# Kernel tuning notes

Hardware: AMD Instinct MI355X
Metric: run time of the kernel (lower is better)

Reference implementation:

```python
import jax, jax.numpy as jnp
import numpy as np

SIGMA_MIN, SIGMA_MAX = 0.03, 0.35
LAMBDA_GEO = 8.0
COMPAT_SCALE = 0.1
INVALID_W = 0.05
NH, HD = 8, 64
LN_EPS = 1e-5

def _ln(x, g, b):
    m = x.mean(-1, keepdims=True)
    v = ((x - m) ** 2).mean(-1, keepdims=True)
    return (x - m) * jax.lax.rsqrt(v + LN_EPS) * g + b

def setup_inputs() -> dict:
    key = jax.random.key(0)
    ks = jax.random.split(key, 32)
    B, C, H, W = 8, 512, 32, 32
    T, S, D, SIN = 1024, 1024, 512, 512
    s = 0.02
    inp = {
        'front_feat': jax.random.normal(ks[0], (B, C, H, W), jnp.float32),
        'sat_tokens': jax.random.normal(ks[1], (B, S, SIN), jnp.float32),
        'sat_xy': jax.random.uniform(ks[2], (B, S, 2), jnp.float32),
        'front_bev_xy': jax.random.uniform(ks[3], (B, T, 2), jnp.float32),
        'front_bev_valid_mask': jax.random.bernoulli(ks[4], 0.9, (B, T)),
        'front_plucker': jax.random.normal(ks[5], (B, T, 6), jnp.float32),
        'fa_w': jax.random.normal(ks[6], (C, D), jnp.float32) * s,
        'fa_b': jnp.zeros((D,), jnp.float32),
        'fa_g': jnp.ones((D,), jnp.float32),
        'fa_lb': jnp.zeros((D,), jnp.float32),
        'sa_w': jax.random.normal(ks[7], (SIN, D), jnp.float32) * s,
        'sa_b': jnp.zeros((D,), jnp.float32),
        'sa_g': jnp.ones((D,), jnp.float32),
        'sa_lb': jnp.zeros((D,), jnp.float32),
        'q_w': jax.random.normal(ks[8], (D, D), jnp.float32) * s,
        'q_b': jnp.zeros((D,), jnp.float32),
        'k_w': jax.random.normal(ks[9], (D, D), jnp.float32) * s,
        'k_b': jnp.zeros((D,), jnp.float32),
        'v_w': jax.random.normal(ks[10], (D, D), jnp.float32) * s,
        'v_b': jnp.zeros((D,), jnp.float32),
        'pl_w1': jax.random.normal(ks[11], (6, D), jnp.float32) * s,
        'pl_b1': jnp.zeros((D,), jnp.float32),
        'pl_w2': jax.random.normal(ks[12], (D, D), jnp.float32) * s,
        'pl_b2': jnp.zeros((D,), jnp.float32),
        'sig_w': jax.random.normal(ks[13], (D, 1), jnp.float32) * s,
        'sig_b': jnp.zeros((1,), jnp.float32),
        'db_w': jax.random.normal(ks[14], (D, NH), jnp.float32) * s,
        'db_b': jnp.zeros((NH,), jnp.float32),
        'out_w': jax.random.normal(ks[15], (D, C), jnp.float32) * s,
        'out_b': jnp.zeros((C,), jnp.float32),
    }
    return inp

def _forward(front_feat, sat_tokens, sat_xy, front_bev_xy, front_plucker,
             fa_w, fa_b, fa_g, fa_lb, sa_w, sa_b, sa_g, sa_lb,
             q_w, q_b, k_w, k_b, v_w, v_b, pl_w1, pl_b1, pl_w2, pl_b2,
             sig_w, sig_b, db_w, db_b, out_w, out_b, valid_mask):
    B, C, H, W = front_feat.shape
    T = H * W
    D = NH * HD
    front_flat = front_feat.reshape(B, C, T).transpose(0, 2, 1)  # [B,T,C]
    front_embed = _ln(front_flat @ fa_w + fa_b, fa_g, fa_lb)
    pl = jax.nn.silu(front_plucker @ pl_w1 + pl_b1) @ pl_w2 + pl_b2
    context = front_embed + pl
    sat_embed = _ln(sat_tokens @ sa_w + sa_b, sa_g, sa_lb)
    def heads(x):
        return x.reshape(B, -1, NH, HD).transpose(0, 2, 1, 3)  # [B,H,N,d]
    q = heads(front_embed @ q_w + q_b)
    k = heads(sat_embed @ k_w + k_b)
    v = heads(sat_embed @ v_w + v_b)
    compat = jnp.einsum('bhtd,bhsd->bhts', q, k) / jnp.sqrt(jnp.float32(HD))
    compat = COMPAT_SCALE * compat
    sigma = SIGMA_MIN + (SIGMA_MAX - SIGMA_MIN) * jax.nn.sigmoid((context @ sig_w + sig_b)[..., 0])  # [B,T]
    dist2 = ((front_bev_xy[:, :, None, :] - sat_xy[:, None, :, :]) ** 2).sum(-1)  # [B,T,S]
    geo = -LAMBDA_GEO * dist2 / jnp.maximum(sigma[..., None] ** 2, 1e-6)
    sat_logits = compat + geo[:, None]  # [B,H,T,S]
    sat_logits = jnp.where(valid_mask[:, None, :, None], sat_logits, jnp.float32(-10000.0))
    dustbin = (context @ db_w + db_b).transpose(0, 2, 1)[..., None]  # [B,H,T,1]
    logits = jnp.concatenate([sat_logits, dustbin], axis=-1)
    probs = jax.nn.softmax(logits, axis=-1)
    sat_probs, dustbin_prob = probs[..., :-1], probs[..., -1]
    read = jnp.einsum('bhts,bhsd->bhtd', sat_probs, v)
    read = read.transpose(0, 2, 1, 3).reshape(B, T, D)
    read_feat = (read @ out_w + out_b).transpose(0, 2, 1).reshape(B, C, H, W)
    confidence = (1.0 - dustbin_prob).mean(axis=1)  # [B,T]
    conf_feat = confidence.reshape(B, 1, H, W)
    front_feat_out = front_feat + conf_feat * read_feat
    vf = valid_mask.astype(confidence.dtype)
    inv = 1.0 - vf
    invalid_conf = (confidence * inv).sum() / jnp.maximum(inv.sum(), 1.0)
    invalid_conf_loss = invalid_conf * INVALID_W
    return front_feat_out, read_feat, confidence, invalid_conf_loss

def reference(front_feat, sat_tokens, sat_xy, front_bev_xy, front_bev_valid_mask, front_plucker,
              fa_w, fa_b, fa_g, fa_lb, sa_w, sa_b, sa_g, sa_lb,
              q_w, q_b, k_w, k_b, v_w, v_b, pl_w1, pl_b1, pl_w2, pl_b2,
              sig_w, sig_b, db_w, db_b, out_w, out_b):
    return _forward(front_feat, sat_tokens, sat_xy, front_bev_xy, front_plucker,
                    fa_w, fa_b, fa_g, fa_lb, sa_w, sa_b, sa_g, sa_lb,
                    q_w, q_b, k_w, k_b, v_w, v_b, pl_w1, pl_b1, pl_w2, pl_b2,
                    sig_w, sig_b, db_w, db_b, out_w, out_b, front_bev_valid_mask)
```

## Files before the change

kernel.cpp:

```cpp
#include <hip/hip_runtime.h>

typedef unsigned short u16;
typedef __attribute__((ext_vector_type(8))) short short8;
typedef __attribute__((ext_vector_type(4))) float f32x4;

constexpr int B_  = 8;
constexpr int C_  = 512;
constexpr int T_  = 1024;
constexpr int S_  = 1024;
constexpr int D_  = 512;
constexpr int NH_ = 8;
constexpr int BT_ = B_ * T_;
constexpr float INVLN2 = 1.44269504088896340736f;
constexpr float QSCALE2 = 0.0125f * INVLN2;

__device__ __forceinline__ unsigned pack2(float lo, float hi) {
    unsigned r;
    asm("v_cvt_pk_bf16_f32 %0, %1, %2" : "=v"(r) : "v"(lo), "v"(hi));
    return r;
}
__device__ __forceinline__ u16 f2bf(float x) {
    return (u16)pack2(x, x);
}
__device__ __forceinline__ float bf2f(u16 h) {
    union { unsigned u; float f; } v; v.u = ((unsigned)h) << 16;
    return v.f;
}
__device__ __forceinline__ float fexp2(float x) {
    float r;
    asm("v_exp_f32 %0, %1" : "=v"(r) : "v"(x));
    return r;
}

typedef __attribute__((address_space(3))) unsigned int lds_u32;
typedef const __attribute__((address_space(1))) unsigned int glob_u32;
__device__ __forceinline__ void g2l16(void* l, const void* g) {
    __builtin_amdgcn_global_load_lds((glob_u32*)g, (lds_u32*)l, 16, 0, 0);
}

__device__ __forceinline__ int is_valid(const void* mask, int mode, int idx) {
    if (mode == 0) return ((const int*)mask)[idx] != 0;
    if (mode == 1) return ((const float*)mask)[idx] != 0.0f;
    return ((const unsigned char*)mask)[idx] != 0;
}

__global__ __launch_bounds__(256) void prep_k(
    const float* __restrict__ ff, const float* __restrict__ sat,
    const float* __restrict__ pl,
    const float* a0, const float* a1, const float* a2, const float* a3,
    const float* a4, const float* a5, const float* a6, u16* __restrict__ WT,
    u16* __restrict__ ffb, u16* __restrict__ satb,
    const float* __restrict__ plw1, const float* __restrict__ plb1,
    u16* __restrict__ plh,
    const unsigned* __restrict__ maskw, int* __restrict__ mode,
    float* __restrict__ scal) {
    __shared__ float tile[32][33];
    int blk = blockIdx.x, tid = threadIdx.x;
    if (blk < 4096) {
        int t0 = (blk & 31) * 32, c0 = ((blk >> 5) & 15) * 32, b = blk >> 9;
        int tx = tid & 31, ty = tid >> 5;
        const float* ip = ff + (size_t)b * C_ * T_;
        for (int i = ty; i < 32; i += 8)
            tile[i][tx] = ip[(size_t)(c0 + i) * T_ + t0 + tx];
        __syncthreads();
        u16* op = ffb + (size_t)b * T_ * C_;
        for (int i = ty; i < 32; i += 8)
            op[(size_t)(t0 + i) * C_ + c0 + tx] = f2bf(tile[tx][i]);
    } else if (blk < 5888) {
        int idx = blk - 4096;
        const float* srcs[7] = {a0, a1, a2, a3, a4, a5, a6};
        int z = idx >> 8;
        const float* src = srcs[z];
        u16* d = WT + (size_t)z * 512 * 512;
        int k0 = (idx & 15) * 32, n0 = ((idx >> 4) & 15) * 32;
        int tx = tid & 31, ty = tid >> 5;
        for (int i = ty; i < 32; i += 8)
            tile[i][tx] = src[(size_t)(k0 + i) * 512 + n0 + tx];
        __syncthreads();
        for (int i = ty; i < 32; i += 8)
            d[(size_t)(n0 + i) * 512 + k0 + tx] = f2bf(tile[tx][i]);
    } else if (blk < 7936) {
        int i = (blk - 5888) * 256 + tid;
        const float4* p = (const float4*)(sat + (size_t)i * 8);
        float4 a = p[0], b = p[1];
        uint4 o;
        o.x = pack2(a.x, a.y); o.y = pack2(a.z, a.w);
        o.z = pack2(b.x, b.y); o.w = pack2(b.z, b.w);
        *(uint4*)(satb + (size_t)i * 8) = o;
    } else if (blk < 9984) {
        int m = (blk - 7936) * 4 + (tid >> 6);
        int lane = tid & 63;
        float p6[6];
#pragma unroll
        for (int j = 0; j < 6; ++j) p6[j] = pl[(size_t)m * 6 + j];
        int n0 = lane * 8;
        float acc[8];
#pragma unroll
        for (int e = 0; e < 8; ++e) acc[e] = plb1[n0 + e];
#pragma unroll
        for (int j = 0; j < 6; ++j) {
            float4 wv0 = *(const float4*)(plw1 + j * D_ + n0);
            float4 wv1 = *(const float4*)(plw1 + j * D_ + n0 + 4);
            acc[0] += p6[j] * wv0.x; acc[1] += p6[j] * wv0.y;
            acc[2] += p6[j] * wv0.z; acc[3] += p6[j] * wv0.w;
            acc[4] += p6[j] * wv1.x; acc[5] += p6[j] * wv1.y;
            acc[6] += p6[j] * wv1.z; acc[7] += p6[j] * wv1.w;
        }
        uint4 o;
        float s0 = acc[0] / (1.0f + __expf(-acc[0]));
        float s1 = acc[1] / (1.0f + __expf(-acc[1]));
        float s2 = acc[2] / (1.0f + __expf(-acc[2]));
        float s3 = acc[3] / (1.0f + __expf(-acc[3]));
        float s4 = acc[4] / (1.0f + __expf(-acc[4]));
        float s5 = acc[5] / (1.0f + __expf(-acc[5]));
        float s6 = acc[6] / (1.0f + __expf(-acc[6]));
        float s7 = acc[7] / (1.0f + __expf(-acc[7]));
        o.x = pack2(s0, s1); o.y = pack2(s2, s3);
        o.z = pack2(s4, s5); o.w = pack2(s6, s7);
        *(uint4*)(plh + (size_t)m * D_ + n0) = o;
    } else {
        __shared__ int bad_i, bad_f;
        if (tid == 0) { bad_i = 0; bad_f = 0; }
        __syncthreads();
        for (int i = tid; i < 2048; i += 256) {
            unsigned v = maskw[i];
            if (v > 1u) bad_i = 1;
            if (v != 0u && v != 0x3f800000u) bad_f = 1;
        }
        __syncthreads();
        if (tid == 0) {
            *mode = (!bad_i) ? 0 : ((!bad_f) ? 1 : 2);
            scal[0] = 0.0f; scal[1] = 0.0f;
        }
    }
}

__global__ __launch_bounds__(256) void gmm_k(
    const u16* __restrict__ A0, const u16* __restrict__ A1,
    const u16* __restrict__ A2, const u16* __restrict__ A3,
    const u16* __restrict__ Bt0, const u16* __restrict__ Bt1,
    const u16* __restrict__ Bt2, const u16* __restrict__ Bt3,
    const float* __restrict__ bb0, const float* __restrict__ bb1,
    const float* __restrict__ bb2, const float* __restrict__ bb3,
    void* __restrict__ C0v, void* __restrict__ C1v,
    void* __restrict__ C2v, void* __restrict__ C3v,
    int md0, int md1, int md2, int md3,
    const u16* __restrict__ addend,
    const float* __restrict__ ffp, const float* __restrict__ confp,
    float* __restrict__ out1p) {
    __shared__ u16 As[2][4096];
    __shared__ u16 Bs[2][4096];
    int jid = blockIdx.x >> 8;
    int L = blockIdx.x & 255;
    const u16* A    = (jid == 0) ? A0 : (jid == 1) ? A1 : (jid == 2) ? A2 : A3;
    const u16* Bt   = (jid == 0) ? Bt0 : (jid == 1) ? Bt1 : (jid == 2) ? Bt2 : Bt3;
    const float* bias = (jid == 0) ? bb0 : (jid == 1) ? bb1 : (jid == 2) ? bb2 : bb3;
    void* Cv        = (jid == 0) ? C0v : (jid == 1) ? C1v : (jid == 2) ? C2v : C3v;
    int mode        = (jid == 0) ? md0 : (jid == 1) ? md1 : (jid == 2) ? md2 : md3;

    int tid = threadIdx.x, w = tid >> 6, l = tid & 63;
    int lr = l & 15, g = l >> 4;
    int W = (L & 7) * 32 + (L >> 3);
    int m0 = (W >> 2) * 128, n0 = (W & 3) * 128;
    int wr = w >> 1, wc = w & 1;
    int prm = g ^ ((lr >> 1) & 3);

    f32x4 acc[4][4] = {};

    auto stage = [&](int buf, int k0) {
#pragma unroll
        for (int j = 0; j < 2; ++j) {
            int i = tid + 256 * j;
            int row = i >> 2, gg = (i & 3) ^ ((i >> 3) & 3);
            g2l16((char*)As[buf] + (size_t)i * 16,
                  A + (size_t)(m0 + row) * 512 + k0 + gg * 8);
        }
#pragma unroll
        for (int j = 0; j < 2; ++j) {
            int i = tid + 256 * j;
            int col = i >> 2, gg = (i & 3) ^ ((i >> 3) & 3);
            g2l16((char*)Bs[buf] + (size_t)i * 16,
                  Bt + (size_t)(n0 + col) * 512 + k0 + gg * 8);
        }
    };

    stage(0, 0);
    __syncthreads();
    int cur = 0;
    for (int t = 0; t < 16; ++t) {
        if (t < 15) stage(cur ^ 1, (t + 1) * 32);
        const char* Ab = (const char*)As[cur];
        const char* Bb = (const char*)Bs[cur];
        short8 af[4], bf[4];
#pragma unroll
        for (int m = 0; m < 4; ++m)
            af[m] = *(const short8*)(Ab + ((wr * 64 + m * 16 + lr) * 4 + prm) * 16);
#pragma unroll
        for (int n = 0; n < 4; ++n)
            bf[n] = *(const short8*)(Bb + ((wc * 64 + n * 16 + lr) * 4 + prm) * 16);
        __builtin_amdgcn_s_setprio(1);
#pragma unroll
        for (int m = 0; m < 4; ++m)
#pragma unroll
            for (int n = 0; n < 4; ++n)
                acc[m][n] = __builtin_amdgcn_mfma_f32_16x16x32_bf16(
                    af[m], bf[n], acc[m][n], 0, 0, 0);
        __builtin_amdgcn_s_setprio(0);
        __syncthreads();
        cur ^= 1;
    }

    float bs[4];
#pragma unroll
    for (int n = 0; n < 4; ++n) bs[n] = bias[n0 + wc * 64 + n * 16 + lr];

#pragma unroll
    for (int m = 0; m < 4; ++m) {
#pragma unroll
        for (int n = 0; n < 4; ++n) {
            int R0  = m0 + wr * 64 + m * 16 + 4 * g;
            int col = n0 + wc * 64 + n * 16 + lr;
            if (mode == 3) {
                int bbx = R0 >> 10, ss = R0 & 1023, hh = col >> 6, dd = col & 63;
                uint2 pk;
                pk.x = pack2(acc[m][n][0] + bs[n], acc[m][n][1] + bs[n]);
                pk.y = pack2(acc[m][n][2] + bs[n], acc[m][n][3] + bs[n]);
                u16* dst = (u16*)Cv + ((size_t)(bbx * 8 + hh) * 64 + dd) * 1024 + ss;
                *(uint2*)dst = pk;
            } else if (mode == 4) {
                int bbx = R0 >> 10, t0p = R0 & 1023;
                size_t base = (size_t)bbx * C_ * T_ + (size_t)col * T_ + t0p;
                float4 rf;
                rf.x = acc[m][n][0] + bs[n]; rf.y = acc[m][n][1] + bs[n];
                rf.z = acc[m][n][2] + bs[n]; rf.w = acc[m][n][3] + bs[n];
                float4 ffv = *(const float4*)(ffp + base);
                float4 cfv = *(const float4*)(confp + bbx * T_ + t0p);
                float4 o0v;
                o0v.x = ffv.x + cfv.x * rf.x; o0v.y = ffv.y + cfv.y * rf.y;
                o0v.z = ffv.z + cfv.z * rf.z; o0v.w = ffv.w + cfv.w * rf.w;
                *(float4*)(out1p + base) = rf;
                *(float4*)((float*)Cv + base) = o0v;
            } else {
#pragma unroll
                for (int j = 0; j < 4; ++j) {
                    int row = R0 + j;
                    float v = acc[m][n][j] + bs[n];
                    if (mode == 1) v *= QSCALE2;
                    if (mode == 2) v += bf2f(addend[(size_t)row * 512 + col]);
                    ((u16*)Cv)[(size_t)row * 512 + col] = f2bf(v);
                }
            }
        }
    }
}

__global__ __launch_bounds__(256) void ln2_k(
    const u16* __restrict__ X0, const float* __restrict__ g0,
    const float* __restrict__ b0, u16* __restrict__ O0,
    const u16* __restrict__ X1, const float* __restrict__ g1,
    const float* __restrict__ b1, u16* __restrict__ O1) {
    int sel = blockIdx.x >> 13;
    int row = blockIdx.x & 8191;
    const u16* X = sel ? X1 : X0;
    const float* gw = sel ? g1 : g0;
    const float* bw = sel ? b1 : b0;
    u16* out = sel ? O1 : O0;
    int tid = threadIdx.x;
    const unsigned* xr = (const unsigned*)(X + (size_t)row * D_);
    unsigned u = xr[tid];
    float x0 = bf2f((u16)(u & 0xffff)), x1 = bf2f((u16)(u >> 16));
    float s = x0 + x1, sq = x0 * x0 + x1 * x1;
    __shared__ float rs[4], rq[4];
    for (int o = 32; o; o >>= 1) { s += __shfl_down(s, o); sq += __shfl_down(sq, o); }
    int wid = tid >> 6, lane = tid & 63;
    if (lane == 0) { rs[wid] = s; rq[wid] = sq; }
    __syncthreads();
    if (tid == 0) {
        float ts = 0, tq = 0;
        for (int w = 0; w < 4; ++w) { ts += rs[w]; tq += rq[w]; }
        rs[0] = ts; rq[0] = tq;
    }
    __syncthreads();
    float mean = rs[0] * (1.0f / D_);
    float var  = rq[0] * (1.0f / D_) - mean * mean;
    float r = rsqrtf(var + 1e-5f);
    float2 g2 = *(const float2*)(gw + 2 * tid);
    float2 b2 = *(const float2*)(bw + 2 * tid);
    float y0 = (x0 - mean) * r * g2.x + b2.x;
    float y1 = (x1 - mean) * r * g2.y + b2.y;
    ((unsigned*)(out + (size_t)row * D_))[tid] = pack2(y0, y1);
}

__global__ __launch_bounds__(256) void head_k(const u16* __restrict__ ctx,
        const float* __restrict__ sw, const float* __restrict__ sbb,
        const float* __restrict__ dw, const float* __restrict__ dbb,
        float* __restrict__ sig, float* __restrict__ dbo) {
    int w = threadIdx.x >> 6, lane = threadIdx.x & 63;
    int row = blockIdx.x * 4 + w;
    const u16* xr = ctx + (size_t)row * D_;
    short8 xv = *(const short8*)(xr + lane * 8);
    float xs[8];
#pragma unroll
    for (int i = 0; i < 8; ++i) xs[i] = bf2f((u16)xv[i]);
    float4 wa = *(const float4*)(sw + lane * 8);
    float4 wb = *(const float4*)(sw + lane * 8 + 4);
    float sacc = xs[0] * wa.x + xs[1] * wa.y + xs[2] * wa.z + xs[3] * wa.w +
                 xs[4] * wb.x + xs[5] * wb.y + xs[6] * wb.z + xs[7] * wb.w;
    float d_[8] = {};
    const float* dr = dw + (size_t)lane * 8 * NH_;
#pragma unroll
    for (int i = 0; i < 8; ++i)
#pragma unroll
        for (int hh = 0; hh < 8; ++hh) d_[hh] += xs[i] * dr[i * NH_ + hh];
    for (int o = 32; o; o >>= 1) {
        sacc += __shfl_down(sacc, o);
#pragma unroll
        for (int hh = 0; hh < 8; ++hh) d_[hh] += __shfl_down(d_[hh], o);
    }
    if (lane == 0) {
        float z = sacc + sbb[0];
        sig[row] = 0.03f + 0.32f / (1.0f + __expf(-z));
        float* dd = dbo + (size_t)row * NH_;
#pragma unroll
        for (int hh = 0; hh < 8; ++hh) dd[hh] = d_[hh] + dbb[hh];
    }
}

__global__ __launch_bounds__(512) void attn_k(
    const u16* __restrict__ Q, const u16* __restrict__ K,
    const u16* __restrict__ Vt, const float* __restrict__ sig,
    const float* __restrict__ dbl, const float* __restrict__ bev,
    const float* __restrict__ sxy, const void* __restrict__ mask,
    const int* __restrict__ mode, u16* __restrict__ OUT,
    float* __restrict__ dbp) {
    int L = blockIdx.x;
    int W = (L & 7) * 64 + (L >> 3);
    int b = W >> 6, h = (W >> 3) & 7, tblk = W & 7;
    int tid = threadIdx.x, w = tid >> 6, l = tid & 63;
    int lr = l & 15, g = l >> 4;
    int p8 = lr & 7;

    __shared__ u16 Kbuf[2][4096];
    __shared__ u16 Vbuf[2][4096];
    __shared__ float2 SXY[1024];
    __shared__ float  SZ[1024];

    const float2* xp = (const float2*)(sxy + (size_t)b * S_ * 2);
#pragma unroll
    for (int j = 0; j < 2; ++j) {
        int idx = tid + 512 * j;
        float2 v = xp[idx];
        SXY[idx] = make_float2(-2.0f * v.x, -2.0f * v.y);
        SZ[idx] = v.x * v.x + v.y * v.y;
    }

    int trow = b * T_ + tblk * 128 + w * 16 + lr;
    float s_ = sig[trow];
    float bx = bev[(size_t)trow * 2], by = bev[(size_t)trow * 2 + 1];
    float dbv2 = dbl[(size_t)trow * NH_ + h] * INVLN2;
    int md = *mode;
    bool vld = is_valid(mask, md, trow) != 0;
    float grow  = vld ? (-11.5415603271117f / fmaxf(s_ * s_, 1e-6f)) : 0.0f;
    float Abase = vld ? grow * (bx * bx + by * by) : -10000.0f;

    const u16* qp = Q + (size_t)trow * 512 + h * 64 + g * 8;
    short8 q0 = *(const short8*)qp;
    short8 q1 = *(const short8*)(qp + 32);
    if (!vld) { q0 = short8{}; q1 = short8{}; }

    const u16* Kp = K + (size_t)b * S_ * 512 + h * 64;
    const u16* Vp = Vt + (size_t)(b * 8 + h) * 64 * 1024;

    int srow = tid >> 3;
    int gprm = (tid & 7) ^ (srow & 7);
    int sK = ((srow >> 5) & 1) * 32 + ((srow >> 2) & 3) * 8 +
             ((srow >> 4) & 1) * 4 + (srow & 3);

    auto stageKV = [&](int buf, int s0) {
        g2l16((char*)Kbuf[buf] + (size_t)tid * 16,
              Kp + (size_t)(s0 + sK) * 512 + gprm * 8);
        g2l16((char*)Vbuf[buf] + (size_t)tid * 16,
              Vp + (size_t)srow * 1024 + s0 + gprm * 8);
    };

    float m_st = dbv2, l_st = 1.0f;
    f32x4 o0 = {}, o1 = {}, o2 = {}, o3 = {};

    stageKV(0, 0);
    __syncthreads();
    int cur = 0;
    for (int c = 0; c < 16; ++c) {
        int s0c = c * 64;
        if (c < 15) stageKV(cur ^ 1, s0c + 64);

        const char* Kc = (const char*)Kbuf[cur];
        const char* Vc = (const char*)Vbuf[cur];

        f32x4 p[4];
        f32x4 z4 = {};
        __builtin_amdgcn_s_setprio(1);
#pragma unroll
        for (int sub = 0; sub < 4; ++sub) {
            int krow = sub * 16 + lr;
            short8 kf0 = *(const short8*)(Kc + (krow * 8 + (g ^ p8)) * 16);
            short8 kf1 = *(const short8*)(Kc + (krow * 8 + ((4 + g) ^ p8)) * 16);
            p[sub] = __builtin_amdgcn_mfma_f32_16x16x32_bf16(kf0, q0, z4, 0, 0, 0);
            p[sub] = __builtin_amdgcn_mfma_f32_16x16x32_bf16(kf1, q1, p[sub], 0, 0, 0);
        }
        __builtin_amdgcn_s_setprio(0);

        float pe[16];
        float cmax = -3.0e38f;
#pragma unroll
        for (int sub = 0; sub < 4; ++sub) {
            int sl = s0c + ((sub & 2) << 4) + 8 * g + ((sub & 1) << 2);
            float4 xy01 = *(const float4*)&SXY[sl];
            float4 xy23 = *(const float4*)&SXY[sl + 2];
            float4 zz   = *(const float4*)&SZ[sl];
            float X[4] = {xy01.x, xy01.z, xy23.x, xy23.z};
            float Y[4] = {xy01.y, xy01.w, xy23.y, xy23.w};
            float Z[4] = {zz.x, zz.y, zz.z, zz.w};
#pragma unroll
            for (int i2 = 0; i2 < 4; ++i2) {
                float wg = fmaf(bx, X[i2], fmaf(by, Y[i2], Z[i2]));
                float lg = fmaf(grow, wg, p[sub][i2] + Abase);
                pe[sub * 4 + i2] = lg;
                cmax = fmaxf(cmax, lg);
            }
        }
        cmax = fmaxf(cmax, __shfl_xor(cmax, 16));
        cmax = fmaxf(cmax, __shfl_xor(cmax, 32));

        if (!__all(cmax <= m_st + 11.5f)) {
            float m_new = fmaxf(m_st, cmax);
            float scl = fexp2(m_st - m_new);
            l_st *= scl;
            o0 *= scl; o1 *= scl; o2 *= scl; o3 *= scl;
            m_st = m_new;
        }
        float ps = 0.0f;
#pragma unroll
        for (int r = 0; r < 16; ++r) { pe[r] = fexp2(pe[r] - m_st); ps += pe[r]; }
        ps += __shfl_xor(ps, 16);
        ps += __shfl_xor(ps, 32);
        l_st += ps;

        union { uint4 u; short8 s8; } pf0, pf1;
        pf0.u.x = pack2(pe[0], pe[1]);  pf0.u.y = pack2(pe[2], pe[3]);
        pf0.u.z = pack2(pe[4], pe[5]);  pf0.u.w = pack2(pe[6], pe[7]);
        pf1.u.x = pack2(pe[8], pe[9]);  pf1.u.y = pack2(pe[10], pe[11]);
        pf1.u.z = pack2(pe[12], pe[13]); pf1.u.w = pack2(pe[14], pe[15]);

        __builtin_amdgcn_s_setprio(1);
        short8 vf;
#pragma unroll
        for (int dt = 0; dt < 4; ++dt) {
            int vrow = dt * 16 + lr;
            f32x4* oo = (dt == 0) ? &o0 : (dt == 1) ? &o1 : (dt == 2) ? &o2 : &o3;
            vf = *(const short8*)(Vc + (vrow * 8 + (g ^ p8)) * 16);
            *oo = __builtin_amdgcn_mfma_f32_16x16x32_bf16(vf, pf0.s8, *oo, 0, 0, 0);
            vf = *(const short8*)(Vc + (vrow * 8 + ((4 + g) ^ p8)) * 16);
            *oo = __builtin_amdgcn_mfma_f32_16x16x32_bf16(vf, pf1.s8, *oo, 0, 0, 0);
        }
        __builtin_amdgcn_s_setprio(0);

        __syncthreads();
        cur ^= 1;
    }

    float inv = 1.0f / l_st;
    u16* ob = OUT + (size_t)trow * 512 + h * 64;
    {
        uint2 pk;
        pk.x = pack2(o0[0] * inv, o0[1] * inv); pk.y = pack2(o0[2] * inv, o0[3] * inv);
        *(uint2*)(ob + 0 * 16 + 4 * g) = pk;
        pk.x = pack2(o1[0] * inv, o1[1] * inv); pk.y = pack2(o1[2] * inv, o1[3] * inv);
        *(uint2*)(ob + 1 * 16 + 4 * g) = pk;
        pk.x = pack2(o2[0] * inv, o2[1] * inv); pk.y = pack2(o2[2] * inv, o2[3] * inv);
        *(uint2*)(ob + 2 * 16 + 4 * g) = pk;
        pk.x = pack2(o3[0] * inv, o3[1] * inv); pk.y = pack2(o3[2] * inv, o3[3] * inv);
        *(uint2*)(ob + 3 * 16 + 4 * g) = pk;
    }
    if (g == 0) dbp[(size_t)trow * NH_ + h] = fexp2(dbv2 - m_st) * inv;
}

__global__ __launch_bounds__(256) void conf_k(const float* __restrict__ dbp,
                                              const void* __restrict__ mask,
                                              const int* __restrict__ mode,
                                              float* __restrict__ confout,
                                              float* __restrict__ scal) {
    int row = blockIdx.x * 256 + threadIdx.x;
    const float* dr = dbp + (size_t)row * NH_;
    float s = 0;
#pragma unroll
    for (int h = 0; h < 8; ++h) s += dr[h];
    float cf = 1.0f - s * (1.0f / NH_);
    confout[row] = cf;
    int md = *mode;
    float inv = is_valid(mask, md, row) ? 0.0f : 1.0f;
    float a = cf * inv, bs = inv;
    __shared__ float ra[4], rb[4];
    for (int o = 32; o; o >>= 1) { a += __shfl_down(a, o); bs += __shfl_down(bs, o); }
    int wid = threadIdx.x >> 6, lane = threadIdx.x & 63;
    if (lane == 0) { ra[wid] = a; rb[wid] = bs; }
    __syncthreads();
    if (threadIdx.x == 0) {
        float ta = 0, tb = 0;
        for (int w = 0; w < 4; ++w) { ta += ra[w]; tb += rb[w]; }
        atomicAdd(&scal[0], ta);
        atomicAdd(&scal[1], tb);
    }
}

__global__ void loss_k(const float* __restrict__ scal, float* __restrict__ out) {
    out[0] = scal[0] / fmaxf(scal[1], 1.0f) * 0.05f;
}

extern "C" void kernel_launch(void* const* d_in, const int* in_sizes, int n_in,
                              void* d_out, int out_size, void* d_ws, size_t ws_size,
                              hipStream_t stream) {
    const float* front_feat = (const float*)d_in[0];
    const float* sat_tokens = (const float*)d_in[1];
    const float* sat_xy     = (const float*)d_in[2];
    const float* bev_xy     = (const float*)d_in[3];
    const void*  mask       = d_in[4];
    const float* plucker    = (const float*)d_in[5];
    const float* fa_w = (const float*)d_in[6];
    const float* fa_b = (const float*)d_in[7];
    const float* fa_g = (const float*)d_in[8];
    const float* fa_lb = (const float*)d_in[9];
    const float* sa_w = (const float*)d_in[10];
    const float* sa_b = (const float*)d_in[11];
    const float* sa_g = (const float*)d_in[12];
    const float* sa_lb = (const float*)d_in[13];
    const float* q_w = (const float*)d_in[14];
    const float* q_b = (const float*)d_in[15];
    const float* k_w = (const float*)d_in[16];
    const float* k_b = (const float*)d_in[17];
    const float* v_w = (const float*)d_in[18];
    const float* v_b = (const float*)d_in[19];
    const float* pl_w1 = (const float*)d_in[20];
    const float* pl_b1 = (const float*)d_in[21];
    const float* pl_w2 = (const float*)d_in[22];
    const float* pl_b2 = (const float*)d_in[23];
    const float* sig_w = (const float*)d_in[24];
    const float* sig_b = (const float*)d_in[25];
    const float* db_w = (const float*)d_in[26];
    const float* db_b = (const float*)d_in[27];
    const float* out_w = (const float*)d_in[28];
    const float* out_b = (const float*)d_in[29];

    char* w8 = (char*)d_ws;
    u16* H0 = (u16*)(w8);
    u16* H1 = (u16*)(w8 + 8388608ull * 1);
    u16* H2 = (u16*)(w8 + 8388608ull * 2);
    u16* H3 = (u16*)(w8 + 8388608ull * 3);
    u16* H4 = (u16*)(w8 + 8388608ull * 4);
    u16* H5 = (u16*)(w8 + 8388608ull * 5);
    u16* H6 = (u16*)(w8 + 8388608ull * 6);
    u16* WT = (u16*)(w8 + 8388608ull * 7);
    char* sm = w8 + 8388608ull * 7 + 3670016ull;
    float* w_sigma = (float*)sm;
    float* w_db    = w_sigma + BT_;
    float* w_dbp   = w_db + (size_t)BT_ * NH_;
    float* w_scal  = w_dbp + (size_t)BT_ * NH_;
    int*   w_mode  = (int*)(w_scal + 2);

    u16* Wfa = WT;                 u16* Wpl2 = WT + 262144ull * 1;
    u16* Wq  = WT + 262144ull * 2; u16* Wsa  = WT + 262144ull * 3;
    u16* Wk  = WT + 262144ull * 4; u16* Wv   = WT + 262144ull * 5;
    u16* Wo  = WT + 262144ull * 6;

    float* out0 = (float*)d_out;
    float* out1 = out0 + (size_t)B_ * C_ * T_;
    float* outc = out1 + (size_t)B_ * C_ * T_;
    float* outl = outc + (size_t)B_ * T_;

    dim3 blk(256);

    prep_k<<<dim3(9985), blk, 0, stream>>>(
        front_feat, sat_tokens, plucker,
        fa_w, pl_w2, q_w, sa_w, k_w, v_w, out_w, WT,
        H0, H5, pl_w1, pl_b1, H2,
        (const unsigned*)mask, w_mode, w_scal);
    gmm_k<<<dim3(512), blk, 0, stream>>>(
        H0, H5, nullptr, nullptr,
        Wfa, Wsa, nullptr, nullptr,
        fa_b, sa_b, nullptr, nullptr,
        H6, H4, nullptr, nullptr,
        0, 0, 0, 0,
        nullptr, nullptr, nullptr, nullptr);
    ln2_k<<<dim3(16384), blk, 0, stream>>>(H6, fa_g, fa_lb, H1,
                                           H4, sa_g, sa_lb, H3);
    gmm_k<<<dim3(1024), blk, 0, stream>>>(
        H1, H2, H3, H3,
        Wq, Wpl2, Wk, Wv,
        q_b, pl_b2, k_b, v_b,
        H5, H6, H0, H4,
        1, 2, 0, 3,
        H1, nullptr, nullptr, nullptr);
    head_k<<<dim3(BT_ / 4), blk, 0, stream>>>(H6, sig_w, sig_b, db_w, db_b,
                                              w_sigma, w_db);
    attn_k<<<dim3(512), dim3(512), 0, stream>>>(
        H5, H0, H4, w_sigma, w_db, bev_xy, sat_xy, mask, w_mode, H2, w_dbp);
    conf_k<<<dim3(BT_ / 256), blk, 0, stream>>>(w_dbp, mask, w_mode, outc, w_scal);
    gmm_k<<<dim3(256), blk, 0, stream>>>(
        H2, nullptr, nullptr, nullptr,
        Wo, nullptr, nullptr, nullptr,
        out_b, nullptr, nullptr, nullptr,
        out0, nullptr, nullptr, nullptr,
        4, 0, 0, 0,
        nullptr, front_feat, outc, out1);
    loss_k<<<1, 1, 0, stream>>>(w_scal, outl);
}
```

Measured before the change: 165.7 us.

## Fuse confidence reduction into output GEMM and simplify attention softmax bookkeeping

The separate conf_k launch is removed. The output GEMM now computes per-row confidence into shared memory, writes the confidence output, and does the masked loss atomics from one column-block per row tile. In the attention kernel, the running max now starts at the dustbin logit, which is folded into the base term, and rescaling only happens when a logit exceeds a threshold. The row sum is taken with an extra MFMA against a ones vector instead of shuffle reductions, and v_max3 is used for the local max. This cuts one launch and some VALU and shuffle work, but adds two MFMAs per tile and accumulates the denominator from bf16-rounded probabilities.

Result: no change. 163.3 us (-1.4%).

```diff
diff --git a/kernel.cpp b/kernel.cpp
--- a/kernel.cpp
+++ b/kernel.cpp
@@ -29,6 +29,11 @@
 __device__ __forceinline__ float fexp2(float x) {
     float r;
     asm("v_exp_f32 %0, %1" : "=v"(r) : "v"(x));
+    return r;
+}
+__device__ __forceinline__ float max3f(float a, float b, float c) {
+    float r;
+    asm("v_max3_f32 %0, %1, %2, %3" : "=v"(r) : "v"(a), "v"(b), "v"(c));
     return r;
 }
 
@@ -146,10 +151,13 @@
     void* __restrict__ C2v, void* __restrict__ C3v,
     int md0, int md1, int md2, int md3,
     const u16* __restrict__ addend,
-    const float* __restrict__ ffp, const float* __restrict__ confp,
-    float* __restrict__ out1p) {
+    const float* __restrict__ ffp, float* __restrict__ out1p,
+    const float* __restrict__ dbpp, const void* __restrict__ maskp,
+    const int* __restrict__ modep, float* __restrict__ outcp,
+    float* __restrict__ scalp) {
     __shared__ u16 As[2][4096];
     __shared__ u16 Bs[2][4096];
+    __shared__ float confL[128];
     int jid = blockIdx.x >> 8;
     int L = blockIdx.x & 255;
     const u16* A    = (jid == 0) ? A0 : (jid == 1) ? A1 : (jid == 2) ? A2 : A3;
@@ -185,6 +193,31 @@
     };
 
     stage(0, 0);
+
+    if (mode == 4 && tid < 128) {
+        int row = m0 + tid;
+        const float* dr = dbpp + (size_t)row * NH_;
+        float s = 0;
+#pragma unroll
+        for (int h = 0; h < 8; ++h) s += dr[h];
+        float cf = 1.0f - s * 0.125f;
+        confL[tid] = cf;
+        if ((W & 3) == 0) {
+            outcp[row] = cf;
+            int md = *modep;
+            float invd = is_valid(maskp, md, row) ? 0.0f : 1.0f;
+            float a = cf * invd, bsum = invd;
+            for (int o = 32; o; o >>= 1) {
+                a += __shfl_down(a, o);
+                bsum += __shfl_down(bsum, o);
+            }
+            if ((tid & 63) == 0) {
+                atomicAdd(&scalp[0], a);
+                atomicAdd(&scalp[1], bsum);
+            }
+        }
+    }
+
     __syncthreads();
     int cur = 0;
     for (int t = 0; t < 16; ++t) {
@@ -234,7 +267,7 @@
                 rf.x = acc[m][n][0] + bs[n]; rf.y = acc[m][n][1] + bs[n];
                 rf.z = acc[m][n][2] + bs[n]; rf.w = acc[m][n][3] + bs[n];
                 float4 ffv = *(const float4*)(ffp + base);
-                float4 cfv = *(const float4*)(confp + bbx * T_ + t0p);
+                float4 cfv = *(const float4*)&confL[R0 - m0];
                 float4 o0v;
                 o0v.x = ffv.x + cfv.x * rf.x; o0v.y = ffv.y + cfv.y * rf.y;
                 o0v.z = ffv.z + cfv.z * rf.z; o0v.w = ffv.w + cfv.w * rf.w;
@@ -362,11 +395,17 @@
     bool vld = is_valid(mask, md, trow) != 0;
     float grow  = vld ? (-11.5415603271117f / fmaxf(s_ * s_, 1e-6f)) : 0.0f;
     float Abase = vld ? grow * (bx * bx + by * by) : -10000.0f;
+    float AbaseM = Abase - dbv2;
+    float mshift = 0.0f;
 
     const u16* qp = Q + (size_t)trow * 512 + h * 64 + g * 8;
     short8 q0 = *(const short8*)qp;
     short8 q1 = *(const short8*)(qp + 32);
     if (!vld) { q0 = short8{}; q1 = short8{}; }
+
+    short8 ones;
+#pragma unroll
+    for (int e = 0; e < 8; ++e) ones[e] = (short)0x3F80;
 
     const u16* Kp = K + (size_t)b * S_ * 512 + h * 64;
     const u16* Vp = Vt + (size_t)(b * 8 + h) * 64 * 1024;
@@ -383,8 +422,8 @@
               Vp + (size_t)srow * 1024 + s0 + gprm * 8);
     };
 
-    float m_st = dbv2, l_st = 1.0f;
     f32x4 o0 = {}, o1 = {}, o2 = {}, o3 = {};
+    f32x4 o4 = {1.0f, 1.0f, 1.0f, 1.0f};
 
     stageKV(0, 0);
     __syncthreads();
@@ -409,8 +448,7 @@
         }
         __builtin_amdgcn_s_setprio(0);
 
-        float pe[16];
-        float cmax = -3.0e38f;
+        float lg[16];
 #pragma unroll
         for (int sub = 0; sub < 4; ++sub) {
             int sl = s0c + ((sub & 2) << 4) + 8 * g + ((sub & 1) << 2);
@@ -423,27 +461,30 @@
 #pragma unroll
             for (int i2 = 0; i2 < 4; ++i2) {
                 float wg = fmaf(bx, X[i2], fmaf(by, Y[i2], Z[i2]));
-                float lg = fmaf(grow, wg, p[sub][i2] + Abase);
-                pe[sub * 4 + i2] = lg;
-                cmax = fmaxf(cmax, lg);
+                lg[sub * 4 + i2] = fmaf(grow, wg, p[sub][i2] + AbaseM);
             }
         }
-        cmax = fmaxf(cmax, __shfl_xor(cmax, 16));
-        cmax = fmaxf(cmax, __shfl_xor(cmax, 32));
-
-        if (!__all(cmax <= m_st + 11.5f)) {
-            float m_new = fmaxf(m_st, cmax);
-            float scl = fexp2(m_st - m_new);
-            l_st *= scl;
-            o0 *= scl; o1 *= scl; o2 *= scl; o3 *= scl;
-            m_st = m_new;
-        }
-        float ps = 0.0f;
-#pragma unroll
-        for (int r = 0; r < 16; ++r) { pe[r] = fexp2(pe[r] - m_st); ps += pe[r]; }
-        ps += __shfl_xor(ps, 16);
-        ps += __shfl_xor(ps, 32);
-        l_st += ps;
+        float c0 = max3f(lg[0], lg[1], lg[2]);
+        float c1 = max3f(lg[3], lg[4], lg[5]);
+        float c2 = max3f(lg[6], lg[7], lg[8]);
+        float c3 = max3f(lg[9], lg[10], lg[11]);
+        float c4 = max3f(lg[12], lg[13], lg[14]);
+        float cl = fmaxf(max3f(c0, c1, c2), max3f(c3, c4, lg[15]));
+
+        if (!__all(cl <= 11.5f)) {
+            cl = fmaxf(cl, __shfl_xor(cl, 16));
+            cl = fmaxf(cl, __shfl_xor(cl, 32));
+            float dm = fmaxf(cl, 0.0f);
+            float scl = fexp2(-dm);
+            o0 *= scl; o1 *= scl; o2 *= scl; o3 *= scl; o4 *= scl;
+            AbaseM -= dm;
+            mshift -= dm;
+#pragma unroll
+            for (int r = 0; r < 16; ++r) lg[r] -= dm;
+        }
+        float pe[16];
+#pragma unroll
+        for (int r = 0; r < 16; ++r) pe[r] = fexp2(lg[r]);
 
         union { uint4 u; short8 s8; } pf0, pf1;
         pf0.u.x = pack2(pe[0], pe[1]);  pf0.u.y = pack2(pe[2], pe[3]);
@@ -462,13 +503,15 @@
             vf = *(const short8*)(Vc + (vrow * 8 + ((4 + g) ^ p8)) * 16);
             *oo = __builtin_amdgcn_mfma_f32_16x16x32_bf16(vf, pf1.s8, *oo, 0, 0, 0);
         }
+        o4 = __builtin_amdgcn_mfma_f32_16x16x32_bf16(ones, pf0.s8, o4, 0, 0, 0);
+        o4 = __builtin_amdgcn_mfma_f32_16x16x32_bf16(ones, pf1.s8, o4, 0, 0, 0);
         __builtin_amdgcn_s_setprio(0);
 
         __syncthreads();
         cur ^= 1;
     }
 
-    float inv = 1.0f / l_st;
+    float inv = 1.0f / o4[0];
     u16* ob = OUT + (size_t)trow * 512 + h * 64;
     {
         uint2 pk;
@@ -481,35 +524,7 @@
         pk.x = pack2(o3[0] * inv, o3[1] * inv); pk.y = pack2(o3[2] * inv, o3[3] * inv);
         *(uint2*)(ob + 3 * 16 + 4 * g) = pk;
     }
-    if (g == 0) dbp[(size_t)trow * NH_ + h] = fexp2(dbv2 - m_st) * inv;
-}
-
-__global__ __launch_bounds__(256) void conf_k(const float* __restrict__ dbp,
-                                              const void* __restrict__ mask,
-                                              const int* __restrict__ mode,
-                                              float* __restrict__ confout,
-                                              float* __restrict__ scal) {
-    int row = blockIdx.x * 256 + threadIdx.x;
-    const float* dr = dbp + (size_t)row * NH_;
-    float s = 0;
-#pragma unroll
-    for (int h = 0; h < 8; ++h) s += dr[h];
-    float cf = 1.0f - s * (1.0f / NH_);
-    confout[row] = cf;
-    int md = *mode;
-    float inv = is_valid(mask, md, row) ? 0.0f : 1.0f;
-    float a = cf * inv, bs = inv;
-    __shared__ float ra[4], rb[4];
-    for (int o = 32; o; o >>= 1) { a += __shfl_down(a, o); bs += __shfl_down(bs, o); }
-    int wid = threadIdx.x >> 6, lane = threadIdx.x & 63;
-    if (lane == 0) { ra[wid] = a; rb[wid] = bs; }
-    __syncthreads();
-    if (threadIdx.x == 0) {
-        float ta = 0, tb = 0;
-        for (int w = 0; w < 4; ++w) { ta += ra[w]; tb += rb[w]; }
-        atomicAdd(&scal[0], ta);
-        atomicAdd(&scal[1], tb);
-    }
+    if (g == 0) dbp[(size_t)trow * NH_ + h] = fexp2(mshift) * inv;
 }
 
 __global__ void loss_k(const float* __restrict__ scal, float* __restrict__ out) {
@@ -589,7 +604,8 @@
         fa_b, sa_b, nullptr, nullptr,
         H6, H4, nullptr, nullptr,
         0, 0, 0, 0,
-        nullptr, nullptr, nullptr, nullptr);
+        nullptr, nullptr, nullptr,
+        nullptr, nullptr, nullptr, nullptr, nullptr);
     ln2_k<<<dim3(16384), blk, 0, stream>>>(H6, fa_g, fa_lb, H1,
                                            H4, sa_g, sa_lb, H3);
     gmm_k<<<dim3(1024), blk, 0, stream>>>(
@@ -598,18 +614,19 @@
         q_b, pl_b2, k_b, v_b,
         H5, H6, H0, H4,
         1, 2, 0, 3,
-        H1, nullptr, nullptr, nullptr);
+        H1, nullptr, nullptr,
+        nullptr, nullptr, nullptr, nullptr, nullptr);
     head_k<<<dim3(BT_ / 4), blk, 0, stream>>>(H6, sig_w, sig_b, db_w, db_b,
                                               w_sigma, w_db);
     attn_k<<<dim3(512), dim3(512), 0, stream>>>(
         H5, H0, H4, w_sigma, w_db, bev_xy, sat_xy, mask, w_mode, H2, w_dbp);
-    conf_k<<<dim3(BT_ / 256), blk, 0, stream>>>(w_dbp, mask, w_mode, outc, w_scal);
     gmm_k<<<dim3(256), blk, 0, stream>>>(
         H2, nullptr, nullptr, nullptr,
         Wo, nullptr, nullptr, nullptr,
         out_b, nullptr, nullptr, nullptr,
         out0, nullptr, nullptr, nullptr,
         4, 0, 0, 0,
-        nullptr, front_feat, outc, out1);
+        nullptr, front_feat, out1,
+        w_dbp, mask, w_mode, outc, w_scal);
     loss_k<<<1, 1, 0, stream>>>(w_scal, outl);
 }
```
